# Performance work log

Measured on AMD Instinct MI355X. Metric: run time of the kernel, lower is better.

Reference implementation:

```python
import jax, jax.numpy as jnp
import numpy as np

N, K = 4096, 256          # rays, samples per ray
V = 100000                # voxel table size
D = 64                    # field MLP hidden dim
SCALER = 7.0              # free-energy scaler from the source


def setup_inputs() -> dict:
    key = jax.random.key(0)
    ks = jax.random.split(key, 12)
    ray_start = jax.random.normal(ks[0], (N, 3), jnp.float32)
    rd = jax.random.normal(ks[1], (N, 3), jnp.float32)
    ray_dir = rd / jnp.linalg.norm(rd, axis=-1, keepdims=True)
    sampled_depth = jnp.sort(
        0.5 + 4.0 * jax.random.uniform(ks[2], (N, K), jnp.float32), axis=-1)
    sampled_dists = 0.02 * jax.random.uniform(ks[3], (N, K), jnp.float32)
    raw = jax.random.randint(ks[4], (N, K), 0, V + V // 4)
    sampled_idx = jnp.where(raw < V, raw, -1).astype(jnp.int64)
    voxel_color = 0.1 * jax.random.normal(ks[5], (V, 3), jnp.float32)
    W1 = jax.random.normal(ks[6], (6, D), jnp.float32) * (1.0 / np.sqrt(6.0))
    b1 = jnp.zeros((D,), jnp.float32)
    w_sigma = jax.random.normal(ks[7], (D, 1), jnp.float32) * (1.0 / np.sqrt(D))
    b_sigma = jnp.zeros((1,), jnp.float32)
    W_tex = jax.random.normal(ks[8], (D, 3), jnp.float32) * (1.0 / np.sqrt(D))
    b_tex = jnp.zeros((3,), jnp.float32)
    return dict(ray_start=ray_start, ray_dir=ray_dir,
                sampled_depth=sampled_depth, sampled_dists=sampled_dists,
                sampled_idx=sampled_idx, voxel_color=voxel_color,
                W1=W1, b1=b1, w_sigma=w_sigma, b_sigma=b_sigma,
                W_tex=W_tex, b_tex=b_tex)


def reference(ray_start, ray_dir, sampled_depth, sampled_dists, sampled_idx,
              voxel_color, W1, b1, w_sigma, b_sigma, W_tex, b_tex):
    mask = sampled_idx != -1                                   # [N,K] sample_mask
    # sampled_xyz = ray(start, dir, depth); sampled_dir broadcast of ray_dir
    xyz = ray_start[:, None, :] + ray_dir[:, None, :] * sampled_depth[..., None]
    dirs = jnp.broadcast_to(ray_dir[:, None, :], xyz.shape)    # [N,K,3]
    feat = jnp.concatenate([xyz, dirs], axis=-1)               # [N,K,6]
    # field_fn: small MLP -> sigma, texture
    h = jax.nn.relu(jnp.einsum('nkf,fd->nkd', feat, W1) + b1)  # [N,K,D]
    sigma = (jnp.einsum('nkd,do->nko', h, w_sigma) + b_sigma)[..., 0]  # [N,K]
    # voxel color embedding lookup (F.embedding); res=True adds it to texture
    idx_safe = jnp.where(mask, sampled_idx, 0)
    vcol = voxel_color[idx_safe]                               # [N,K,3] gather
    texture = jnp.einsum('nkd,dc->nkc', h, W_tex) + b_tex + vcol
    # free energy; masked_scatter == zero-out where mask is False
    free_energy = jnp.where(mask,
                            jax.nn.relu(sigma) * sampled_dists * SCALER, 0.0)
    texture = jnp.where(mask[..., None], texture, 0.0)
    # alpha compositing: a = 1-exp(-fe), b = exp(-cumsum(shifted fe))
    shifted = jnp.concatenate(
        [jnp.zeros((free_energy.shape[0], 1), free_energy.dtype),
         free_energy[:, :-1]], axis=-1)
    a = 1.0 - jnp.exp(-free_energy)
    b = jnp.exp(-jnp.cumsum(shifted, axis=-1))
    probs = a * b                                              # [N,K]
    depths = jnp.sum(sampled_depth * probs, axis=-1)           # [N]
    missed = 1.0 - jnp.sum(probs, axis=-1)                     # [N]
    colors = jnp.sum(texture * probs[..., None], axis=-2)      # [N,3]
    return colors, depths, missed, probs
```

## Files before the change

kernel.cpp:

```cpp
#include <hip/hip_runtime.h>

#define K_SAMP 256
#define D_HID 64
#define SCALER_FE 7.0f

typedef _Float16 half8  __attribute__((ext_vector_type(8)));
typedef __fp16   fp16x2 __attribute__((ext_vector_type(2)));
typedef float    f32x4  __attribute__((ext_vector_type(4)));

union H8U4 { half8 h; uint4 u; };
union H8P  { fp16x2 h2[4]; half8 h8; };

__device__ __forceinline__ half8 h8zero() {
    half8 a;
    #pragma unroll
    for (int j = 0; j < 8; ++j) a[j] = (_Float16)0.f;
    return a;
}

#define DPP_ADD(x, ctrl, rowmask)                                              \
    (x) += __int_as_float(__builtin_amdgcn_update_dpp(                         \
        0, __float_as_int(x), (ctrl), (rowmask), 0xf, false))

__device__ __forceinline__ float dpp_scan_incl(float x) {
    DPP_ADD(x, 0x111, 0xf);
    DPP_ADD(x, 0x112, 0xf);
    DPP_ADD(x, 0x114, 0xf);
    DPP_ADD(x, 0x118, 0xf);
    DPP_ADD(x, 0x142, 0xa);
    DPP_ADD(x, 0x143, 0xc);
    return x;
}

__global__ __launch_bounds__(256, 4)
void volrend_kernel(const float* __restrict__ ray_start,
                    const float* __restrict__ ray_dir,
                    const float* __restrict__ depth,
                    const float* __restrict__ dists,
                    const int*   __restrict__ vidx,
                    const float* __restrict__ vcol_tab,
                    const float* __restrict__ W1,
                    const float* __restrict__ b1,
                    const float* __restrict__ w_sigma,
                    const float* __restrict__ b_sigma,
                    const float* __restrict__ W_tex,
                    const float* __restrict__ b_tex,
                    float* __restrict__ out_colors,
                    float* __restrict__ out_depths,
                    float* __restrict__ out_missed,
                    float* __restrict__ out_probs) {
    __shared__ uint4 sFrag[6 * 64];
    __shared__ float sOut[4][K_SAMP][4];

    const int tid  = threadIdx.x;
    const int lane = tid & 63;
    const int wv   = tid >> 6;
    const int ray  = __builtin_amdgcn_readfirstlane(blockIdx.x * 4 + wv);
    const int m    = lane & 15;
    const int g    = lane >> 4;

    if (tid < 64) {
        #pragma unroll
        for (int tt = 0; tt < 4; ++tt) {
            const int dim = 8 * (m >> 2) + (m & 3) + 4 * (tt & 1) + 32 * (tt >> 1);
            half8 a = h8zero();
            if (g == 0) {
                #pragma unroll
                for (int j = 0; j < 6; ++j) a[j] = (_Float16)W1[j * D_HID + dim];
                a[6] = (_Float16)b1[dim];
            }
            H8U4 c; c.h = a;
            sFrag[tt * 64 + lane] = c.u;
        }
        half8 a2a = h8zero(), a2b = h8zero();
        if (m < 4) {
            const int c = (m >= 1) ? (m - 1) : 0;
            #pragma unroll
            for (int j = 0; j < 8; ++j) {
                const int d = 8 * g + j;
                a2a[j] = (_Float16)((m == 0) ? w_sigma[d]      : W_tex[d * 3 + c]);
                a2b[j] = (_Float16)((m == 0) ? w_sigma[d + 32] : W_tex[(d + 32) * 3 + c]);
            }
        }
        H8U4 ca; ca.h = a2a; sFrag[4 * 64 + lane] = ca.u;
        H8U4 cb; cb.h = a2b; sFrag[5 * 64 + lane] = cb.u;
    }

    const float rs0 = ray_start[ray * 3 + 0];
    const float rs1 = ray_start[ray * 3 + 1];
    const float rs2 = ray_start[ray * 3 + 2];
    const float rd0 = ray_dir[ray * 3 + 0];
    const float rd1 = ray_dir[ray * 3 + 1];
    const float rd2 = ray_dir[ray * 3 + 2];
    const float bs  = b_sigma[0];
    const float bt0 = b_tex[0], bt1 = b_tex[1], bt2 = b_tex[2];

    const size_t rayBase = (size_t)ray * K_SAMP;
    const float4 dep4 = ((const float4*)(depth + rayBase))[lane];
    const float4 dst4 = ((const float4*)(dists + rayBase))[lane];
    const int4   vi4  = ((const int4*)(vidx  + rayBase))[lane];
    const int via[4] = {vi4.x, vi4.y, vi4.z, vi4.w};
    bool  msk[4];
    float vc[4][3];
    #pragma unroll
    for (int s = 0; s < 4; ++s) {
        msk[s] = (via[s] != -1);
        const int b = (msk[s] ? via[s] : 0) * 3;
        vc[s][0] = vcol_tab[b + 0];
        vc[s][1] = vcol_tab[b + 1];
        vc[s][2] = vcol_tab[b + 2];
    }

    __syncthreads();

    half8 a1[4];
    #pragma unroll
    for (int tt = 0; tt < 4; ++tt) { H8U4 c; c.u = sFrag[tt * 64 + lane]; a1[tt] = c.h; }
    H8U4 ca; ca.u = sFrag[4 * 64 + lane]; const half8 a2a = ca.h;
    H8U4 cb; cb.u = sFrag[5 * 64 + lane]; const half8 a2b = cb.h;

    f32x4 oinit = {0.f, 0.f, 0.f, 0.f};
    if (g == 0) { oinit[0] = bs; oinit[1] = bt0; oinit[2] = bt1; oinit[3] = bt2; }
    const f32x4 zero4 = {0.f, 0.f, 0.f, 0.f};

    const fp16x2 hc12 = __builtin_amdgcn_cvt_pkrtz(rd1, rd2);
    const fp16x2 hc3  = __builtin_amdgcn_cvt_pkrtz(1.0f, 0.0f);

    #pragma unroll 4
    for (int t = 0; t < 16; ++t) {
        const float dpt = depth[rayBase + 16 * t + m];
        const float fx = fmaf(rd0, dpt, rs0);
        const float fy = fmaf(rd1, dpt, rs1);
        const float fz = fmaf(rd2, dpt, rs2);
        H8P bb;
        bb.h2[0] = __builtin_amdgcn_cvt_pkrtz(fx, fy);
        bb.h2[1] = __builtin_amdgcn_cvt_pkrtz(fz, rd0);
        bb.h2[2] = hc12;
        bb.h2[3] = hc3;
        const f32x4 h0 = __builtin_amdgcn_mfma_f32_16x16x32_f16(a1[0], bb.h8, zero4, 0, 0, 0);
        const f32x4 h1 = __builtin_amdgcn_mfma_f32_16x16x32_f16(a1[1], bb.h8, zero4, 0, 0, 0);
        const f32x4 h2 = __builtin_amdgcn_mfma_f32_16x16x32_f16(a1[2], bb.h8, zero4, 0, 0, 0);
        const f32x4 h3 = __builtin_amdgcn_mfma_f32_16x16x32_f16(a1[3], bb.h8, zero4, 0, 0, 0);

        H8P p2a, p2b;
        p2a.h2[0] = __builtin_amdgcn_cvt_pkrtz(fmaxf(h0[0], 0.f), fmaxf(h0[1], 0.f));
        p2a.h2[1] = __builtin_amdgcn_cvt_pkrtz(fmaxf(h0[2], 0.f), fmaxf(h0[3], 0.f));
        p2a.h2[2] = __builtin_amdgcn_cvt_pkrtz(fmaxf(h1[0], 0.f), fmaxf(h1[1], 0.f));
        p2a.h2[3] = __builtin_amdgcn_cvt_pkrtz(fmaxf(h1[2], 0.f), fmaxf(h1[3], 0.f));
        p2b.h2[0] = __builtin_amdgcn_cvt_pkrtz(fmaxf(h2[0], 0.f), fmaxf(h2[1], 0.f));
        p2b.h2[1] = __builtin_amdgcn_cvt_pkrtz(fmaxf(h2[2], 0.f), fmaxf(h2[3], 0.f));
        p2b.h2[2] = __builtin_amdgcn_cvt_pkrtz(fmaxf(h3[0], 0.f), fmaxf(h3[1], 0.f));
        p2b.h2[3] = __builtin_amdgcn_cvt_pkrtz(fmaxf(h3[2], 0.f), fmaxf(h3[3], 0.f));

        f32x4 o = oinit;
        o = __builtin_amdgcn_mfma_f32_16x16x32_f16(a2a, p2a.h8, o, 0, 0, 0);
        o = __builtin_amdgcn_mfma_f32_16x16x32_f16(a2b, p2b.h8, o, 0, 0, 0);

        if (g == 0) {
            *(float4*)&sOut[wv][16 * t + m][0] = make_float4(o[0], o[1], o[2], o[3]);
        }
    }

    const float depa[4] = {dep4.x, dep4.y, dep4.z, dep4.w};
    const float dsta[4] = {dst4.x, dst4.y, dst4.z, dst4.w};
    float fe[4], tA[4], tB[4], tC[4];
    #pragma unroll
    for (int s = 0; s < 4; ++s) {
        const float4 r4 = *(const float4*)&sOut[wv][4 * lane + s][0];
        if (msk[s]) {
            fe[s] = fmaxf(r4.x, 0.f) * dsta[s] * SCALER_FE;
            tA[s] = r4.y + vc[s][0];
            tB[s] = r4.z + vc[s][1];
            tC[s] = r4.w + vc[s][2];
        } else {
            fe[s] = 0.f; tA[s] = 0.f; tB[s] = 0.f; tC[s] = 0.f;
        }
    }

    const float T = fe[0] + fe[1] + fe[2] + fe[3];
    const float x = dpp_scan_incl(T);
    const float e0 = x - T;
    const float e1 = e0 + fe[0];
    const float e2 = e1 + fe[1];
    const float e3 = e2 + fe[2];

    const float p0 = (1.0f - __expf(-fe[0])) * __expf(-e0);
    const float p1 = (1.0f - __expf(-fe[1])) * __expf(-e1);
    const float p2 = (1.0f - __expf(-fe[2])) * __expf(-e2);
    const float p3 = (1.0f - __expf(-fe[3])) * __expf(-e3);

    ((float4*)(out_probs + rayBase))[lane] = make_float4(p0, p1, p2, p3);

    float sp = dpp_scan_incl(p0 + p1 + p2 + p3);
    float sd = dpp_scan_incl(depa[0] * p0 + depa[1] * p1 + depa[2] * p2 + depa[3] * p3);
    float c0 = dpp_scan_incl(tA[0] * p0 + tA[1] * p1 + tA[2] * p2 + tA[3] * p3);
    float c1 = dpp_scan_incl(tB[0] * p0 + tB[1] * p1 + tB[2] * p2 + tB[3] * p3);
    float c2 = dpp_scan_incl(tC[0] * p0 + tC[1] * p1 + tC[2] * p2 + tC[3] * p3);
    if (lane == 63) {
        out_colors[ray * 3 + 0] = c0;
        out_colors[ray * 3 + 1] = c1;
        out_colors[ray * 3 + 2] = c2;
        out_depths[ray] = sd;
        out_missed[ray] = 1.0f - sp;
    }
}

extern "C" void kernel_launch(void* const* d_in, const int* in_sizes, int n_in,
                              void* d_out, int out_size, void* d_ws, size_t ws_size,
                              hipStream_t stream) {
    const float* ray_start  = (const float*)d_in[0];
    const float* ray_dir    = (const float*)d_in[1];
    const float* depth      = (const float*)d_in[2];
    const float* dists      = (const float*)d_in[3];
    const int*   vidx       = (const int*)d_in[4];
    const float* vcol       = (const float*)d_in[5];
    const float* W1         = (const float*)d_in[6];
    const float* b1         = (const float*)d_in[7];
    const float* w_sigma    = (const float*)d_in[8];
    const float* b_sigma    = (const float*)d_in[9];
    const float* W_tex      = (const float*)d_in[10];
    const float* b_tex      = (const float*)d_in[11];

    const int N = in_sizes[0] / 3;
    float* out        = (float*)d_out;
    float* out_colors = out;
    float* out_depths = out + (size_t)N * 3;
    float* out_missed = out + (size_t)N * 3 + N;
    float* out_probs  = out + (size_t)N * 3 + 2 * (size_t)N;

    volrend_kernel<<<N / 4, 256, 0, stream>>>(
        ray_start, ray_dir, depth, dists, vidx, vcol,
        W1, b1, w_sigma, b_sigma, W_tex, b_tex,
        out_colors, out_depths, out_missed, out_probs);
}
```

Baseline: 19.39 us.

## Use strided sample ownership and planar LDS layouts for scan and staging

Changes sample-to-lane mapping from 4 contiguous samples per lane to lane+64*s striding, so each global load and probs store is a scalar coalesced access. LDS staging buffers switch from float4-interleaved to planar arrays, likely to avoid bank conflicts on the strided reads. The prefix sum now needs four separate DPP scans plus four cross-lane broadcasts instead of one, which adds cross-lane work in exchange for the layout change.

```diff
diff --git a/kernel.cpp b/kernel.cpp
--- a/kernel.cpp
+++ b/kernel.cpp
@@ -8,8 +8,8 @@
 typedef __fp16   fp16x2 __attribute__((ext_vector_type(2)));
 typedef float    f32x4  __attribute__((ext_vector_type(4)));
 
-union H8U4 { half8 h; uint4 u; };
-union H8P  { fp16x2 h2[4]; half8 h8; };
+union H8U { half8 h; uint u[4]; };
+union H8P { fp16x2 h2[4]; half8 h8; };
 
 __device__ __forceinline__ half8 h8zero() {
     half8 a;
@@ -49,8 +49,8 @@
                     float* __restrict__ out_depths,
                     float* __restrict__ out_missed,
                     float* __restrict__ out_probs) {
-    __shared__ uint4 sFrag[6 * 64];
-    __shared__ float sOut[4][K_SAMP][4];
+    __shared__ uint  sFragP[4][6 * 64];
+    __shared__ float sOutP[4][4 * K_SAMP];
 
     const int tid  = threadIdx.x;
     const int lane = tid & 63;
@@ -69,8 +69,9 @@
                 for (int j = 0; j < 6; ++j) a[j] = (_Float16)W1[j * D_HID + dim];
                 a[6] = (_Float16)b1[dim];
             }
-            H8U4 c; c.h = a;
-            sFrag[tt * 64 + lane] = c.u;
+            H8U c; c.h = a;
+            #pragma unroll
+            for (int k = 0; k < 4; ++k) sFragP[k][tt * 64 + lane] = c.u[k];
         }
         half8 a2a = h8zero(), a2b = h8zero();
         if (m < 4) {
@@ -82,8 +83,13 @@
                 a2b[j] = (_Float16)((m == 0) ? w_sigma[d + 32] : W_tex[(d + 32) * 3 + c]);
             }
         }
-        H8U4 ca; ca.h = a2a; sFrag[4 * 64 + lane] = ca.u;
-        H8U4 cb; cb.h = a2b; sFrag[5 * 64 + lane] = cb.u;
+        H8U ca; ca.h = a2a;
+        H8U cb; cb.h = a2b;
+        #pragma unroll
+        for (int k = 0; k < 4; ++k) {
+            sFragP[k][4 * 64 + lane] = ca.u[k];
+            sFragP[k][5 * 64 + lane] = cb.u[k];
+        }
     }
 
     const float rs0 = ray_start[ray * 3 + 0];
@@ -96,16 +102,21 @@
     const float bt0 = b_tex[0], bt1 = b_tex[1], bt2 = b_tex[2];
 
     const size_t rayBase = (size_t)ray * K_SAMP;
-    const float4 dep4 = ((const float4*)(depth + rayBase))[lane];
-    const float4 dst4 = ((const float4*)(dists + rayBase))[lane];
-    const int4   vi4  = ((const int4*)(vidx  + rayBase))[lane];
-    const int via[4] = {vi4.x, vi4.y, vi4.z, vi4.w};
+    float dep_[4], dst_[4];
+    int   vi_[4];
+    #pragma unroll
+    for (int s = 0; s < 4; ++s) {
+        const int n = lane + 64 * s;
+        dep_[s] = depth[rayBase + n];
+        dst_[s] = dists[rayBase + n];
+        vi_[s]  = vidx[rayBase + n];
+    }
     bool  msk[4];
     float vc[4][3];
     #pragma unroll
     for (int s = 0; s < 4; ++s) {
-        msk[s] = (via[s] != -1);
-        const int b = (msk[s] ? via[s] : 0) * 3;
+        msk[s] = (vi_[s] != -1);
+        const int b = (msk[s] ? vi_[s] : 0) * 3;
         vc[s][0] = vcol_tab[b + 0];
         vc[s][1] = vcol_tab[b + 1];
         vc[s][2] = vcol_tab[b + 2];
@@ -115,9 +126,20 @@
 
     half8 a1[4];
     #pragma unroll
-    for (int tt = 0; tt < 4; ++tt) { H8U4 c; c.u = sFrag[tt * 64 + lane]; a1[tt] = c.h; }
-    H8U4 ca; ca.u = sFrag[4 * 64 + lane]; const half8 a2a = ca.h;
-    H8U4 cb; cb.u = sFrag[5 * 64 + lane]; const half8 a2b = cb.h;
+    for (int tt = 0; tt < 4; ++tt) {
+        H8U c;
+        #pragma unroll
+        for (int k = 0; k < 4; ++k) c.u[k] = sFragP[k][tt * 64 + lane];
+        a1[tt] = c.h;
+    }
+    H8U ca, cb;
+    #pragma unroll
+    for (int k = 0; k < 4; ++k) {
+        ca.u[k] = sFragP[k][4 * 64 + lane];
+        cb.u[k] = sFragP[k][5 * 64 + lane];
+    }
+    const half8 a2a = ca.h;
+    const half8 a2b = cb.h;
 
     f32x4 oinit = {0.f, 0.f, 0.f, 0.f};
     if (g == 0) { oinit[0] = bs; oinit[1] = bt0; oinit[2] = bt1; oinit[3] = bt2; }
@@ -157,45 +179,57 @@
         o = __builtin_amdgcn_mfma_f32_16x16x32_f16(a2b, p2b.h8, o, 0, 0, 0);
 
         if (g == 0) {
-            *(float4*)&sOut[wv][16 * t + m][0] = make_float4(o[0], o[1], o[2], o[3]);
-        }
-    }
-
-    const float depa[4] = {dep4.x, dep4.y, dep4.z, dep4.w};
-    const float dsta[4] = {dst4.x, dst4.y, dst4.z, dst4.w};
-    float fe[4], tA[4], tB[4], tC[4];
-    #pragma unroll
-    for (int s = 0; s < 4; ++s) {
-        const float4 r4 = *(const float4*)&sOut[wv][4 * lane + s][0];
+            const int idx = (wv << 8) + 16 * t + m;
+            sOutP[0][idx] = o[0];
+            sOutP[1][idx] = o[1];
+            sOutP[2][idx] = o[2];
+            sOutP[3][idx] = o[3];
+        }
+    }
+
+    float fe_[4], tA[4], tB[4], tC[4];
+    #pragma unroll
+    for (int s = 0; s < 4; ++s) {
+        const int idx = (wv << 8) + lane + 64 * s;
+        const float sg = sOutP[0][idx];
+        const float u0 = sOutP[1][idx];
+        const float u1 = sOutP[2][idx];
+        const float u2 = sOutP[3][idx];
         if (msk[s]) {
-            fe[s] = fmaxf(r4.x, 0.f) * dsta[s] * SCALER_FE;
-            tA[s] = r4.y + vc[s][0];
-            tB[s] = r4.z + vc[s][1];
-            tC[s] = r4.w + vc[s][2];
+            fe_[s] = fmaxf(sg, 0.f) * dst_[s] * SCALER_FE;
+            tA[s] = u0 + vc[s][0];
+            tB[s] = u1 + vc[s][1];
+            tC[s] = u2 + vc[s][2];
         } else {
-            fe[s] = 0.f; tA[s] = 0.f; tB[s] = 0.f; tC[s] = 0.f;
-        }
-    }
-
-    const float T = fe[0] + fe[1] + fe[2] + fe[3];
-    const float x = dpp_scan_incl(T);
-    const float e0 = x - T;
-    const float e1 = e0 + fe[0];
-    const float e2 = e1 + fe[1];
-    const float e3 = e2 + fe[2];
-
-    const float p0 = (1.0f - __expf(-fe[0])) * __expf(-e0);
-    const float p1 = (1.0f - __expf(-fe[1])) * __expf(-e1);
-    const float p2 = (1.0f - __expf(-fe[2])) * __expf(-e2);
-    const float p3 = (1.0f - __expf(-fe[3])) * __expf(-e3);
-
-    ((float4*)(out_probs + rayBase))[lane] = make_float4(p0, p1, p2, p3);
-
-    float sp = dpp_scan_incl(p0 + p1 + p2 + p3);
-    float sd = dpp_scan_incl(depa[0] * p0 + depa[1] * p1 + depa[2] * p2 + depa[3] * p3);
-    float c0 = dpp_scan_incl(tA[0] * p0 + tA[1] * p1 + tA[2] * p2 + tA[3] * p3);
-    float c1 = dpp_scan_incl(tB[0] * p0 + tB[1] * p1 + tB[2] * p2 + tB[3] * p3);
-    float c2 = dpp_scan_incl(tC[0] * p0 + tC[1] * p1 + tC[2] * p2 + tC[3] * p3);
+            fe_[s] = 0.f; tA[s] = 0.f; tB[s] = 0.f; tC[s] = 0.f;
+        }
+    }
+
+    float incl[4], tot[4];
+    #pragma unroll
+    for (int s = 0; s < 4; ++s) incl[s] = dpp_scan_incl(fe_[s]);
+    #pragma unroll
+    for (int s = 0; s < 4; ++s) tot[s] = __shfl(incl[s], 63, 64);
+
+    float p_[4];
+    float base = 0.f;
+    #pragma unroll
+    for (int s = 0; s < 4; ++s) {
+        const float e = base + incl[s] - fe_[s];
+        p_[s] = (1.0f - __expf(-fe_[s])) * __expf(-e);
+        base += tot[s];
+    }
+    #pragma unroll
+    for (int s = 0; s < 4; ++s) {
+        out_probs[rayBase + lane + 64 * s] = p_[s];
+    }
+
+    float sp = dpp_scan_incl(p_[0] + p_[1] + p_[2] + p_[3]);
+    float sd = dpp_scan_incl(dep_[0] * p_[0] + dep_[1] * p_[1] +
+                             dep_[2] * p_[2] + dep_[3] * p_[3]);
+    float c0 = dpp_scan_incl(tA[0] * p_[0] + tA[1] * p_[1] + tA[2] * p_[2] + tA[3] * p_[3]);
+    float c1 = dpp_scan_incl(tB[0] * p_[0] + tB[1] * p_[1] + tB[2] * p_[2] + tB[3] * p_[3]);
+    float c2 = dpp_scan_incl(tC[0] * p_[0] + tC[1] * p_[1] + tC[2] * p_[2] + tC[3] * p_[3]);
     if (lane == 63) {
         out_colors[ray * 3 + 0] = c0;
         out_colors[ray * 3 + 1] = c1;
```

New measurement: 19.88 us. +2.5%, slower.

## Fuse compositing into MFMA loop with one-wave blocks and no LDS

Applied to the files above, without the earlier changes.

Switches to one 64-thread block per ray. Each wave now builds its own MLP weight fragments in registers, so the shared-memory staging and the barrier are gone. Free energy, the row-wise DPP prefix scan, the probabilities and the color and depth accumulation are computed inside the per-tile MFMA loop, replacing the LDS round trip and the end-of-kernel scans. In exchange, every block reloads the weights from global memory. Only 16 lanes hold valid results, so three quarters of the lanes do redundant transcendental work, and the probs stores are narrower scalar writes.

```diff
diff --git a/kernel.cpp b/kernel.cpp
--- a/kernel.cpp
+++ b/kernel.cpp
@@ -8,8 +8,7 @@
 typedef __fp16   fp16x2 __attribute__((ext_vector_type(2)));
 typedef float    f32x4  __attribute__((ext_vector_type(4)));
 
-union H8U4 { half8 h; uint4 u; };
-union H8P  { fp16x2 h2[4]; half8 h8; };
+union H8P { fp16x2 h2[4]; half8 h8; };
 
 __device__ __forceinline__ half8 h8zero() {
     half8 a;
@@ -18,21 +17,11 @@
     return a;
 }
 
-#define DPP_ADD(x, ctrl, rowmask)                                              \
+#define DPP_ADD(x, ctrl)                                                       \
     (x) += __int_as_float(__builtin_amdgcn_update_dpp(                         \
-        0, __float_as_int(x), (ctrl), (rowmask), 0xf, false))
+        0, __float_as_int(x), (ctrl), 0xf, 0xf, false))
 
-__device__ __forceinline__ float dpp_scan_incl(float x) {
-    DPP_ADD(x, 0x111, 0xf);
-    DPP_ADD(x, 0x112, 0xf);
-    DPP_ADD(x, 0x114, 0xf);
-    DPP_ADD(x, 0x118, 0xf);
-    DPP_ADD(x, 0x142, 0xa);
-    DPP_ADD(x, 0x143, 0xc);
-    return x;
-}
-
-__global__ __launch_bounds__(256, 4)
+__global__ __launch_bounds__(64, 4)
 void volrend_kernel(const float* __restrict__ ray_start,
                     const float* __restrict__ ray_dir,
                     const float* __restrict__ depth,
@@ -49,42 +38,10 @@
                     float* __restrict__ out_depths,
                     float* __restrict__ out_missed,
                     float* __restrict__ out_probs) {
-    __shared__ uint4 sFrag[6 * 64];
-    __shared__ float sOut[4][K_SAMP][4];
-
-    const int tid  = threadIdx.x;
-    const int lane = tid & 63;
-    const int wv   = tid >> 6;
-    const int ray  = __builtin_amdgcn_readfirstlane(blockIdx.x * 4 + wv);
+    const int lane = threadIdx.x;
+    const int ray  = __builtin_amdgcn_readfirstlane(blockIdx.x);
     const int m    = lane & 15;
     const int g    = lane >> 4;
-
-    if (tid < 64) {
-        #pragma unroll
-        for (int tt = 0; tt < 4; ++tt) {
-            const int dim = 8 * (m >> 2) + (m & 3) + 4 * (tt & 1) + 32 * (tt >> 1);
-            half8 a = h8zero();
-            if (g == 0) {
-                #pragma unroll
-                for (int j = 0; j < 6; ++j) a[j] = (_Float16)W1[j * D_HID + dim];
-                a[6] = (_Float16)b1[dim];
-            }
-            H8U4 c; c.h = a;
-            sFrag[tt * 64 + lane] = c.u;
-        }
-        half8 a2a = h8zero(), a2b = h8zero();
-        if (m < 4) {
-            const int c = (m >= 1) ? (m - 1) : 0;
-            #pragma unroll
-            for (int j = 0; j < 8; ++j) {
-                const int d = 8 * g + j;
-                a2a[j] = (_Float16)((m == 0) ? w_sigma[d]      : W_tex[d * 3 + c]);
-                a2b[j] = (_Float16)((m == 0) ? w_sigma[d + 32] : W_tex[(d + 32) * 3 + c]);
-            }
-        }
-        H8U4 ca; ca.h = a2a; sFrag[4 * 64 + lane] = ca.u;
-        H8U4 cb; cb.h = a2b; sFrag[5 * 64 + lane] = cb.u;
-    }
 
     const float rs0 = ray_start[ray * 3 + 0];
     const float rs1 = ray_start[ray * 3 + 1];
@@ -95,29 +52,28 @@
     const float bs  = b_sigma[0];
     const float bt0 = b_tex[0], bt1 = b_tex[1], bt2 = b_tex[2];
 
-    const size_t rayBase = (size_t)ray * K_SAMP;
-    const float4 dep4 = ((const float4*)(depth + rayBase))[lane];
-    const float4 dst4 = ((const float4*)(dists + rayBase))[lane];
-    const int4   vi4  = ((const int4*)(vidx  + rayBase))[lane];
-    const int via[4] = {vi4.x, vi4.y, vi4.z, vi4.w};
-    bool  msk[4];
-    float vc[4][3];
-    #pragma unroll
-    for (int s = 0; s < 4; ++s) {
-        msk[s] = (via[s] != -1);
-        const int b = (msk[s] ? via[s] : 0) * 3;
-        vc[s][0] = vcol_tab[b + 0];
-        vc[s][1] = vcol_tab[b + 1];
-        vc[s][2] = vcol_tab[b + 2];
-    }
-
-    __syncthreads();
-
     half8 a1[4];
     #pragma unroll
-    for (int tt = 0; tt < 4; ++tt) { H8U4 c; c.u = sFrag[tt * 64 + lane]; a1[tt] = c.h; }
-    H8U4 ca; ca.u = sFrag[4 * 64 + lane]; const half8 a2a = ca.h;
-    H8U4 cb; cb.u = sFrag[5 * 64 + lane]; const half8 a2b = cb.h;
+    for (int tt = 0; tt < 4; ++tt) {
+        const int dim = 8 * (m >> 2) + (m & 3) + 4 * (tt & 1) + 32 * (tt >> 1);
+        half8 a = h8zero();
+        if (g == 0) {
+            #pragma unroll
+            for (int j = 0; j < 6; ++j) a[j] = (_Float16)W1[j * D_HID + dim];
+            a[6] = (_Float16)b1[dim];
+        }
+        a1[tt] = a;
+    }
+    half8 a2a = h8zero(), a2b = h8zero();
+    if (m < 4) {
+        const int c = (m >= 1) ? (m - 1) : 0;
+        #pragma unroll
+        for (int j = 0; j < 8; ++j) {
+            const int d = 8 * g + j;
+            a2a[j] = (_Float16)((m == 0) ? w_sigma[d]      : W_tex[d * 3 + c]);
+            a2b[j] = (_Float16)((m == 0) ? w_sigma[d + 32] : W_tex[(d + 32) * 3 + c]);
+        }
+    }
 
     f32x4 oinit = {0.f, 0.f, 0.f, 0.f};
     if (g == 0) { oinit[0] = bs; oinit[1] = bt0; oinit[2] = bt1; oinit[3] = bt2; }
@@ -126,9 +82,15 @@
     const fp16x2 hc12 = __builtin_amdgcn_cvt_pkrtz(rd1, rd2);
     const fp16x2 hc3  = __builtin_amdgcn_cvt_pkrtz(1.0f, 0.0f);
 
-    #pragma unroll 4
+    const size_t rayBase = (size_t)ray * K_SAMP;
+
+    float S = 0.f;
+    float accP = 0.f, accD = 0.f, accC0 = 0.f, accC1 = 0.f, accC2 = 0.f;
+
+    #pragma unroll 2
     for (int t = 0; t < 16; ++t) {
-        const float dpt = depth[rayBase + 16 * t + m];
+        const int  n   = 16 * t + m;
+        const float dpt = depth[rayBase + n];
         const float fx = fmaf(rd0, dpt, rs0);
         const float fy = fmaf(rd1, dpt, rs1);
         const float fz = fmaf(rd2, dpt, rs2);
@@ -156,52 +118,50 @@
         o = __builtin_amdgcn_mfma_f32_16x16x32_f16(a2a, p2a.h8, o, 0, 0, 0);
         o = __builtin_amdgcn_mfma_f32_16x16x32_f16(a2b, p2b.h8, o, 0, 0, 0);
 
-        if (g == 0) {
-            *(float4*)&sOut[wv][16 * t + m][0] = make_float4(o[0], o[1], o[2], o[3]);
-        }
+        const float dstv = dists[rayBase + n];
+        const int   viv  = vidx[rayBase + n];
+        const bool  mk   = (viv != -1);
+        const int   vb   = (mk ? viv : 0) * 3;
+        const float vc0  = vcol_tab[vb + 0];
+        const float vc1  = vcol_tab[vb + 1];
+        const float vc2  = vcol_tab[vb + 2];
+
+        const float fe = mk ? fmaxf(o[0], 0.f) * dstv * SCALER_FE : 0.f;
+        float incl = fe;
+        DPP_ADD(incl, 0x111);
+        DPP_ADD(incl, 0x112);
+        DPP_ADD(incl, 0x114);
+        DPP_ADD(incl, 0x118);
+        const float rowtot =
+            __int_as_float(__builtin_amdgcn_readlane(__float_as_int(incl), 15));
+        const float eB = S + incl;
+        const float eA = eB - fe;
+        const float p  = __expf(-eA) - __expf(-eB);
+        S += rowtot;
+
+        if (g == 0) out_probs[rayBase + n] = p;
+
+        const float tA = mk ? o[1] + vc0 : 0.f;
+        const float tB = mk ? o[2] + vc1 : 0.f;
+        const float tC = mk ? o[3] + vc2 : 0.f;
+        accP += p;
+        accD  = fmaf(dpt, p, accD);
+        accC0 = fmaf(tA,  p, accC0);
+        accC1 = fmaf(tB,  p, accC1);
+        accC2 = fmaf(tC,  p, accC2);
     }
 
-    const float depa[4] = {dep4.x, dep4.y, dep4.z, dep4.w};
-    const float dsta[4] = {dst4.x, dst4.y, dst4.z, dst4.w};
-    float fe[4], tA[4], tB[4], tC[4];
-    #pragma unroll
-    for (int s = 0; s < 4; ++s) {
-        const float4 r4 = *(const float4*)&sOut[wv][4 * lane + s][0];
-        if (msk[s]) {
-            fe[s] = fmaxf(r4.x, 0.f) * dsta[s] * SCALER_FE;
-            tA[s] = r4.y + vc[s][0];
-            tB[s] = r4.z + vc[s][1];
-            tC[s] = r4.w + vc[s][2];
-        } else {
-            fe[s] = 0.f; tA[s] = 0.f; tB[s] = 0.f; tC[s] = 0.f;
-        }
-    }
-
-    const float T = fe[0] + fe[1] + fe[2] + fe[3];
-    const float x = dpp_scan_incl(T);
-    const float e0 = x - T;
-    const float e1 = e0 + fe[0];
-    const float e2 = e1 + fe[1];
-    const float e3 = e2 + fe[2];
-
-    const float p0 = (1.0f - __expf(-fe[0])) * __expf(-e0);
-    const float p1 = (1.0f - __expf(-fe[1])) * __expf(-e1);
-    const float p2 = (1.0f - __expf(-fe[2])) * __expf(-e2);
-    const float p3 = (1.0f - __expf(-fe[3])) * __expf(-e3);
-
-    ((float4*)(out_probs + rayBase))[lane] = make_float4(p0, p1, p2, p3);
-
-    float sp = dpp_scan_incl(p0 + p1 + p2 + p3);
-    float sd = dpp_scan_incl(depa[0] * p0 + depa[1] * p1 + depa[2] * p2 + depa[3] * p3);
-    float c0 = dpp_scan_incl(tA[0] * p0 + tA[1] * p1 + tA[2] * p2 + tA[3] * p3);
-    float c1 = dpp_scan_incl(tB[0] * p0 + tB[1] * p1 + tB[2] * p2 + tB[3] * p3);
-    float c2 = dpp_scan_incl(tC[0] * p0 + tC[1] * p1 + tC[2] * p2 + tC[3] * p3);
-    if (lane == 63) {
-        out_colors[ray * 3 + 0] = c0;
-        out_colors[ray * 3 + 1] = c1;
-        out_colors[ray * 3 + 2] = c2;
-        out_depths[ray] = sd;
-        out_missed[ray] = 1.0f - sp;
+    DPP_ADD(accP,  0x111); DPP_ADD(accP,  0x112); DPP_ADD(accP,  0x114); DPP_ADD(accP,  0x118);
+    DPP_ADD(accD,  0x111); DPP_ADD(accD,  0x112); DPP_ADD(accD,  0x114); DPP_ADD(accD,  0x118);
+    DPP_ADD(accC0, 0x111); DPP_ADD(accC0, 0x112); DPP_ADD(accC0, 0x114); DPP_ADD(accC0, 0x118);
+    DPP_ADD(accC1, 0x111); DPP_ADD(accC1, 0x112); DPP_ADD(accC1, 0x114); DPP_ADD(accC1, 0x118);
+    DPP_ADD(accC2, 0x111); DPP_ADD(accC2, 0x112); DPP_ADD(accC2, 0x114); DPP_ADD(accC2, 0x118);
+    if (lane == 15) {
+        out_colors[ray * 3 + 0] = accC0;
+        out_colors[ray * 3 + 1] = accC1;
+        out_colors[ray * 3 + 2] = accC2;
+        out_depths[ray] = accD;
+        out_missed[ray] = 1.0f - accP;
     }
 }
 
@@ -228,7 +188,7 @@
     float* out_missed = out + (size_t)N * 3 + N;
     float* out_probs  = out + (size_t)N * 3 + 2 * (size_t)N;
 
-    volrend_kernel<<<N / 4, 256, 0, stream>>>(
+    volrend_kernel<<<N, 64, 0, stream>>>(
         ray_start, ray_dir, depth, dists, vidx, vcol,
         W1, b1, w_sigma, b_sigma, W_tex, b_tex,
         out_colors, out_depths, out_missed, out_probs);
```

After: 22.90 us. +18.1%, slower.
